# Optimization experiments

Hardware: AMD Instinct MI355X
Metric: run time of the kernel (lower is better)

Reference implementation:

```python
import jax, jax.numpy as jnp
import numpy as np

L, H, NH, NKV, HD, FF, E, K = 4, 1024, 16, 4, 64, 2048, 8, 2
B, S = 2, 2048
THETA, EPS = 10000.0, 1e-5


def setup_inputs() -> dict:
    key = jax.random.key(0)
    ks = jax.random.split(key, 12)
    sc = 0.02
    inp = {
        "hidden_states": jax.random.normal(ks[0], (B, S, H), jnp.float32),
        "ln1_w": jnp.ones((L, H), jnp.float32),
        "ln2_w": jnp.ones((L, H), jnp.float32),
        "wq": jax.random.normal(ks[1], (L, H, NH * HD), jnp.float32) * sc,
        "wk": jax.random.normal(ks[2], (L, H, NKV * HD), jnp.float32) * sc,
        "wv": jax.random.normal(ks[3], (L, H, NKV * HD), jnp.float32) * sc,
        "wo": jax.random.normal(ks[4], (L, NH * HD, H), jnp.float32) * sc,
        "wr": jax.random.normal(ks[5], (L, H, E), jnp.float32) * sc,
        "wg": jax.random.normal(ks[6], (L, E, H, FF), jnp.float32) * sc,
        "wu": jax.random.normal(ks[7], (L, E, H, FF), jnp.float32) * sc,
        "wd": jax.random.normal(ks[8], (L, E, FF, H), jnp.float32) * sc,
    }
    return inp


def _rms(x, w):
    return x * jax.lax.rsqrt(jnp.mean(x * x, axis=-1, keepdims=True) + EPS) * w


def _rope_cos_sin(seq_len, head_dim, theta):
    inv = 1.0 / (theta ** (jnp.arange(0, head_dim, 2, dtype=jnp.float32) / head_dim))
    f = jnp.arange(seq_len, dtype=jnp.float32)[:, None] * inv  # [S, HD/2]
    emb = jnp.concatenate([f, f], axis=-1)  # [S, HD]
    return jnp.cos(emb), jnp.sin(emb)


def _rot_half(x):
    h = x.shape[-1] // 2
    return jnp.concatenate([-x[..., h:], x[..., :h]], axis=-1)


def _attention(x, wq, wk, wv, wo, cos, sin, causal_bias):
    b, s, _ = x.shape
    q = (x @ wq).reshape(b, s, NH, HD).transpose(0, 2, 1, 3)   # [B,NH,S,HD]
    k = (x @ wk).reshape(b, s, NKV, HD).transpose(0, 2, 1, 3)  # [B,NKV,S,HD]
    v = (x @ wv).reshape(b, s, NKV, HD).transpose(0, 2, 1, 3)
    c = cos[None, None]
    sn = sin[None, None]
    q = q * c + _rot_half(q) * sn
    k = k * c + _rot_half(k) * sn
    rep = NH // NKV
    k = jnp.repeat(k, rep, axis=1)  # [B,NH,S,HD]
    v = jnp.repeat(v, rep, axis=1)
    scores = jnp.einsum("bhqd,bhkd->bhqk", q, k) / jnp.sqrt(jnp.asarray(HD, x.dtype))
    scores = scores + causal_bias  # [1,1,S,S] broadcast
    attn = jax.nn.softmax(scores, axis=-1)
    out = jnp.einsum("bhqk,bhkd->bhqd", attn, v)
    out = out.transpose(0, 2, 1, 3).reshape(b, s, NH * HD)
    return out @ wo


def _moe(x, wr, wg, wu, wd):
    logits = x @ wr                            # [B,S,E]
    probs = jax.nn.softmax(logits, axis=-1)
    topv, topi = jax.lax.top_k(probs, K)       # [B,S,K]
    topv = topv / jnp.sum(topv, axis=-1, keepdims=True)
    # dense per-expert combine weights [B,S,E]
    comb = jnp.sum(jax.nn.one_hot(topi, E, dtype=x.dtype) * topv[..., None], axis=-2)
    out = jnp.zeros_like(x)
    for e in range(E):  # fixed small expert count
        h = jax.nn.silu(x @ wg[e]) * (x @ wu[e])  # [B,S,FF]
        out = out + comb[..., e:e + 1] * (h @ wd[e])
    return out


def reference(hidden_states, ln1_w, ln2_w, wq, wk, wv, wo, wr, wg, wu, wd):
    s = hidden_states.shape[1]
    cos, sin = _rope_cos_sin(s, HD, THETA)
    causal_bias = jnp.where(
        jnp.tril(jnp.ones((s, s), bool))[None, None], 0.0, -1e9
    ).astype(hidden_states.dtype)
    x = hidden_states
    for l in range(L):
        res = x
        h = _rms(x, ln1_w[l])
        h = _attention(h, wq[l], wk[l], wv[l], wo[l], cos, sin, causal_bias)
        x = jnp.clip(res + h, -100.0, 100.0)
        res = x
        h = _rms(x, ln2_w[l])
        h = _moe(h, wr[l], wg[l], wu[l], wd[l])
        x = jnp.clip(res + h, -100.0, 100.0)
    return x
```

## Files before the change

kernel.cpp:

```cpp
#include <hip/hip_runtime.h>
#include <math.h>

typedef unsigned short u16;
typedef short short8 __attribute__((ext_vector_type(8)));
typedef short short4v __attribute__((ext_vector_type(4)));
typedef float f32x4 __attribute__((ext_vector_type(4)));

#define NLAYER 4
#define HDIM 1024
#define NHEAD 16
#define NKVH 4
#define FFDIM 2048
#define NEXP 8
#define SEQ 2048
#define NBATCH 2
#define NTOK (NBATCH*SEQ)
#define NPAIR (NTOK*2)
#define RMS_EPS 1e-5f

__device__ __forceinline__ u16 b16(float x) {
  unsigned u = __builtin_bit_cast(unsigned, x);
  unsigned r = (u + 0x7FFFu + ((u >> 16) & 1u)) >> 16;
  return (u16)r;
}
__device__ __forceinline__ float b2f(u16 b) {
  return __builtin_bit_cast(float, ((unsigned)b) << 16);
}
__device__ __forceinline__ void split2(float x, u16& o0, u16& o1) {
  o0 = b16(x); o1 = b16(x - b2f(o0));
}
__device__ __forceinline__ float clip100(float v) {
  return fminf(fmaxf(v, -100.f), 100.f);
}
__device__ __forceinline__ int swz8(int bid, int nwg) {
  return (bid & 7) * (nwg >> 3) + (bid >> 3);
}

__global__ __launch_bounds__(256)
void rmsnorm_kernel(const float* __restrict__ x, const float* __restrict__ w,
                    u16* __restrict__ oh, u16* __restrict__ ol) {
  int t = blockIdx.x, tid = threadIdx.x;
  const float* xr = x + (long)t * HDIM;
  float4 v = *(const float4*)(xr + tid * 4);
  float ss = v.x*v.x + v.y*v.y + v.z*v.z + v.w*v.w;
  #pragma unroll
  for (int m = 32; m; m >>= 1) ss += __shfl_xor(ss, m);
  __shared__ float sb[4];
  if ((tid & 63) == 0) sb[tid >> 6] = ss;
  __syncthreads();
  ss = sb[0] + sb[1] + sb[2] + sb[3];
  float sc = 1.0f / sqrtf(ss * (1.f/HDIM) + RMS_EPS);
  float4 wv = *(const float4*)(w + tid * 4);
  float ov[4] = {v.x*sc*wv.x, v.y*sc*wv.y, v.z*sc*wv.z, v.w*sc*wv.w};
  short4v hv, lv;
  #pragma unroll
  for (int j = 0; j < 4; j++) { u16 h, l; split2(ov[j], h, l); hv[j]=(short)h; lv[j]=(short)l; }
  *(short4v*)&oh[(long)t*HDIM + tid*4] = hv;
  *(short4v*)&ol[(long)t*HDIM + tid*4] = lv;
}

__global__ __launch_bounds__(256)
void rope_table_kernel(float* __restrict__ tab) {
  int idx = blockIdx.x * 256 + threadIdx.x;
  int i = idx & 31, pos = idx >> 5;
  double e = -(double)i * 0.28782313662425575;
  float inv = (float)exp(e);
  float f = (float)pos * inv;
  tab[idx] = cosf(f);
  tab[SEQ*32 + idx] = sinf(f);
}

#define GPAD 40

__device__ __forceinline__ void gemm_core(
    const u16* __restrict__ Ah, const u16* __restrict__ Al, long arow,
    const float* __restrict__ Bp, int Nb, int bcol0, int K,
    u16 (&As)[2][256][GPAD], u16 (&Bs)[2][64][GPAD],
    int tid, int wr, int lr, int lg, f32x4 (&acc)[4][4])
{
  int b_col = tid & 63;
  int b_kh = (tid >> 6) * 8;
  short8 pA[8];
  float pB[8];
  short8 cBh, cBl;
  auto loadA = [&](int k0) {
    if (arow >= 0) {
      const u16* ah = Ah + arow * (long)K + k0;
      const u16* al = Al + arow * (long)K + k0;
      #pragma unroll
      for (int q = 0; q < 4; q++) {
        pA[q]     = *(const short8*)(ah + q*8);
        pA[4 + q] = *(const short8*)(al + q*8);
      }
    } else {
      short8 z = {0,0,0,0,0,0,0,0};
      #pragma unroll
      for (int q = 0; q < 8; q++) pA[q] = z;
    }
  };
  auto loadB = [&](int k0) {
    const float* bp = Bp + (long)(k0 + b_kh) * Nb + bcol0 + b_col;
    #pragma unroll
    for (int j = 0; j < 8; j++) pB[j] = bp[(long)j * Nb];
  };
  auto convB = [&]() {
    #pragma unroll
    for (int j = 0; j < 8; j++) {
      u16 h, l; split2(pB[j], h, l);
      cBh[j] = (short)h; cBl[j] = (short)l;
    }
  };
  loadA(0); loadB(0); convB();
  for (int k0 = 0; k0 < K; k0 += 32) {
    if (k0) __syncthreads();
    #pragma unroll
    for (int q = 0; q < 4; q++) {
      *(short8*)&As[0][tid][q*8] = pA[q];
      *(short8*)&As[1][tid][q*8] = pA[4 + q];
    }
    *(short8*)&Bs[0][b_col][b_kh] = cBh;
    *(short8*)&Bs[1][b_col][b_kh] = cBl;
    __syncthreads();
    int kn = k0 + 32;
    if (kn < K) { loadA(kn); loadB(kn); }
    short8 bf[2][4];
    #pragma unroll
    for (int t = 0; t < 2; t++)
      #pragma unroll
      for (int n = 0; n < 4; n++)
        bf[t][n] = *(const short8*)&Bs[t][n*16 + lr][lg*8];
    #pragma unroll
    for (int m = 0; m < 4; m++) {
      short8 afh = *(const short8*)&As[0][wr + m*16 + lr][lg*8];
      short8 afl = *(const short8*)&As[1][wr + m*16 + lr][lg*8];
      #pragma unroll
      for (int n = 0; n < 4; n++) {
        f32x4 a = acc[m][n];
        a = __builtin_amdgcn_mfma_f32_16x16x32_bf16(afh, bf[0][n], a, 0, 0, 0);
        a = __builtin_amdgcn_mfma_f32_16x16x32_bf16(afh, bf[1][n], a, 0, 0, 0);
        a = __builtin_amdgcn_mfma_f32_16x16x32_bf16(afl, bf[0][n], a, 0, 0, 0);
        acc[m][n] = a;
      }
    }
    if (kn < K) convB();
  }
}

__device__ __forceinline__ void gemm_core128(
    const u16* __restrict__ Ah, const u16* __restrict__ Al, long arow,
    const float* __restrict__ Bp, int Nb, int bcol0, int K,
    u16 (&As)[2][128][GPAD], u16 (&Bs)[2][64][GPAD],
    int tid, int wr, int lr, int lg, f32x4 (&acc)[2][4])
{
  int a_r = tid >> 1, a_kq = (tid & 1) * 16;
  int b_col = tid & 63;
  int b_kh = (tid >> 6) * 8;
  short8 pA[4];
  float pB[8];
  short8 cBh, cBl;
  auto loadA = [&](int k0) {
    if (arow >= 0) {
      const u16* ah = Ah + arow * (long)K + k0 + a_kq;
      const u16* al = Al + arow * (long)K + k0 + a_kq;
      pA[0] = *(const short8*)ah;
      pA[1] = *(const short8*)(ah + 8);
      pA[2] = *(const short8*)al;
      pA[3] = *(const short8*)(al + 8);
    } else {
      short8 z = {0,0,0,0,0,0,0,0};
      #pragma unroll
      for (int q = 0; q < 4; q++) pA[q] = z;
    }
  };
  auto loadB = [&](int k0) {
    const float* bp = Bp + (long)(k0 + b_kh) * Nb + bcol0 + b_col;
    #pragma unroll
    for (int j = 0; j < 8; j++) pB[j] = bp[(long)j * Nb];
  };
  auto convB = [&]() {
    #pragma unroll
    for (int j = 0; j < 8; j++) {
      u16 h, l; split2(pB[j], h, l);
      cBh[j] = (short)h; cBl[j] = (short)l;
    }
  };
  loadA(0); loadB(0); convB();
  for (int k0 = 0; k0 < K; k0 += 32) {
    if (k0) __syncthreads();
    *(short8*)&As[0][a_r][a_kq]     = pA[0];
    *(short8*)&As[0][a_r][a_kq + 8] = pA[1];
    *(short8*)&As[1][a_r][a_kq]     = pA[2];
    *(short8*)&As[1][a_r][a_kq + 8] = pA[3];
    *(short8*)&Bs[0][b_col][b_kh] = cBh;
    *(short8*)&Bs[1][b_col][b_kh] = cBl;
    __syncthreads();
    int kn = k0 + 32;
    if (kn < K) { loadA(kn); loadB(kn); }
    short8 bf[2][4];
    #pragma unroll
    for (int t = 0; t < 2; t++)
      #pragma unroll
      for (int n = 0; n < 4; n++)
        bf[t][n] = *(const short8*)&Bs[t][n*16 + lr][lg*8];
    #pragma unroll
    for (int m = 0; m < 2; m++) {
      short8 afh = *(const short8*)&As[0][wr + m*16 + lr][lg*8];
      short8 afl = *(const short8*)&As[1][wr + m*16 + lr][lg*8];
      #pragma unroll
      for (int n = 0; n < 4; n++) {
        f32x4 a = acc[m][n];
        a = __builtin_amdgcn_mfma_f32_16x16x32_bf16(afh, bf[0][n], a, 0, 0, 0);
        a = __builtin_amdgcn_mfma_f32_16x16x32_bf16(afh, bf[1][n], a, 0, 0, 0);
        a = __builtin_amdgcn_mfma_f32_16x16x32_bf16(afl, bf[0][n], a, 0, 0, 0);
        acc[m][n] = a;
      }
    }
    if (kn < K) convB();
  }
}

__global__ __launch_bounds__(256)
void gemm_down(const u16* __restrict__ Ah, const u16* __restrict__ Al,
               const float* __restrict__ B, float* __restrict__ Cf,
               const int* __restrict__ offs, int N, int K, long bstride, int ncol)
{
  __shared__ u16 As[2][128][GPAD];
  __shared__ u16 Bs[2][64][GPAD];
  int nwg = gridDim.x;
  int bid = swz8(blockIdx.x, nwg);
  int cpe = nwg >> 3;
  int z = bid / cpe, rr2 = bid % cpe;
  int rs = offs[z], re = offs[z + 1];
  int brow = rr2 / ncol, bcol = rr2 % ncol;
  int p0 = rs + brow * 128;
  if (p0 >= re) return;
  int bcol0 = bcol * 64;
  const float* Bp = B + (long)z * bstride;
  int tid = threadIdx.x, wv = tid >> 6, lane = tid & 63;
  int lr = lane & 15, lg = lane >> 4;
  int wr = wv * 32;
  long arow = -1;
  { int rr = p0 + (tid >> 1); if (rr < re) arow = rr; }
  f32x4 acc[2][4];
  #pragma unroll
  for (int m = 0; m < 2; m++)
    #pragma unroll
    for (int n = 0; n < 4; n++) acc[m][n] = {0.f,0.f,0.f,0.f};
  gemm_core128(Ah, Al, arow, Bp, N, bcol0, K, As, Bs, tid, wr, lr, lg, acc);
  #pragma unroll
  for (int m = 0; m < 2; m++) {
    int row0 = p0 + wr + m*16 + lg*4;
    #pragma unroll
    for (int n = 0; n < 4; n++) {
      int col = bcol0 + n*16 + lr;
      #pragma unroll
      for (int r = 0; r < 4; r++) {
        int row = row0 + r;
        if (row < re) Cf[(long)row * N + col] = acc[m][n][r];
      }
    }
  }
}

__global__ __launch_bounds__(256)
void gemm_wo(const u16* __restrict__ Ah, const u16* __restrict__ Al,
             const float* __restrict__ B, float* __restrict__ Cf,
             int M, int N, int K, int ncol)
{
  __shared__ u16 As[2][128][GPAD];
  __shared__ u16 Bs[2][64][GPAD];
  int bid = swz8(blockIdx.x, gridDim.x);
  int brow = bid / ncol, bcol = bid % ncol;
  int p0 = brow * 128;
  int bcol0 = bcol * 64;
  int tid = threadIdx.x, wv = tid >> 6, lane = tid & 63;
  int lr = lane & 15, lg = lane >> 4;
  int wr = wv * 32;
  long arow = p0 + (tid >> 1);
  f32x4 acc[2][4];
  #pragma unroll
  for (int m = 0; m < 2; m++)
    #pragma unroll
    for (int n = 0; n < 4; n++) acc[m][n] = {0.f,0.f,0.f,0.f};
  gemm_core128(Ah, Al, arow, B, N, bcol0, K, As, Bs, tid, wr, lr, lg, acc);
  #pragma unroll
  for (int m = 0; m < 2; m++) {
    int row0 = p0 + wr + m*16 + lg*4;
    #pragma unroll
    for (int n = 0; n < 4; n++) {
      int col = bcol0 + n*16 + lr;
      #pragma unroll
      for (int r = 0; r < 4; r++) {
        long idx = (long)(row0 + r) * N + col;
        Cf[idx] = clip100(Cf[idx] + acc[m][n][r]);
      }
    }
  }
}

#define GUPAD 40
__global__ __launch_bounds__(256, 2)
void gemm_gateup(const u16* __restrict__ Ah, const u16* __restrict__ Al,
                 const float* __restrict__ Bg, const float* __restrict__ Bu,
                 u16* __restrict__ Ch, u16* __restrict__ Cl,
                 const int* __restrict__ gather, const int* __restrict__ offs)
{
  __shared__ u16 As[2][256][GUPAD];
  __shared__ u16 Bgs[2][64][GUPAD];
  __shared__ u16 Bus[2][64][GUPAD];
  const int K = HDIM, N = FFDIM;
  int nwg = gridDim.x;
  int bid = swz8(blockIdx.x, nwg);
  int cpe = nwg >> 3;
  int z = bid / cpe, rr2 = bid % cpe;
  int rs = offs[z], re = offs[z + 1];
  int brow = rr2 >> 5, bcol = rr2 & 31;
  int p0 = rs + brow * 256;
  if (p0 >= re) return;
  int bcol0 = bcol * 64;
  const float* Bpg = Bg + (long)z * ((long)HDIM * FFDIM);
  const float* Bpu = Bu + (long)z * ((long)HDIM * FFDIM);
  int tid = threadIdx.x, wv = tid >> 6, lane = tid & 63;
  int lr = lane & 15, lg = lane >> 4;
  int wr = wv * 64;
  long arow = -1;
  { int rr = p0 + tid; if (rr < re) arow = gather[rr]; }
  f32x4 accg[4][4], accu[4][4];
  #pragma unroll
  for (int m = 0; m < 4; m++)
    #pragma unroll
    for (int n = 0; n < 4; n++) { accg[m][n] = {0.f,0.f,0.f,0.f}; accu[m][n] = {0.f,0.f,0.f,0.f}; }
  int b_col = tid & 63;
  int b_kh = (tid >> 6) * 8;
  short8 pA[8];
  float pBg[8], pBu[8];
  short8 cGh, cGl, cUh, cUl;
  auto loadA = [&](int k0) {
    if (arow >= 0) {
      const u16* ah = Ah + arow * (long)K + k0;
      const u16* al = Al + arow * (long)K + k0;
      #pragma unroll
      for (int q = 0; q < 4; q++) {
        pA[q]     = *(const short8*)(ah + q*8);
        pA[4 + q] = *(const short8*)(al + q*8);
      }
    } else {
      short8 zz = {0,0,0,0,0,0,0,0};
      #pragma unroll
      for (int q = 0; q < 8; q++) pA[q] = zz;
    }
  };
  auto loadB = [&](int k0) {
    const float* bpg = Bpg + (long)(k0 + b_kh) * N + bcol0 + b_col;
    const float* bpu = Bpu + (long)(k0 + b_kh) * N + bcol0 + b_col;
    #pragma unroll
    for (int j = 0; j < 8; j++) { pBg[j] = bpg[(long)j * N]; pBu[j] = bpu[(long)j * N]; }
  };
  auto convB = [&]() {
    #pragma unroll
    for (int j = 0; j < 8; j++) {
      u16 h, l;
      split2(pBg[j], h, l); cGh[j] = (short)h; cGl[j] = (short)l;
      split2(pBu[j], h, l); cUh[j] = (short)h; cUl[j] = (short)l;
    }
  };
  loadA(0); loadB(0); convB();
  for (int k0 = 0; k0 < K; k0 += 32) {
    if (k0) __syncthreads();
    #pragma unroll
    for (int q = 0; q < 4; q++) {
      *(short8*)&As[0][tid][q*8] = pA[q];
      *(short8*)&As[1][tid][q*8] = pA[4 + q];
    }
    *(short8*)&Bgs[0][b_col][b_kh] = cGh;
    *(short8*)&Bgs[1][b_col][b_kh] = cGl;
    *(short8*)&Bus[0][b_col][b_kh] = cUh;
    *(short8*)&Bus[1][b_col][b_kh] = cUl;
    __syncthreads();
    int kn = k0 + 32;
    if (kn < K) { loadA(kn); loadB(kn); }
    short8 afh[4], afl[4];
    #pragma unroll
    for (int m = 0; m < 4; m++) {
      afh[m] = *(const short8*)&As[0][wr + m*16 + lr][lg*8];
      afl[m] = *(const short8*)&As[1][wr + m*16 + lr][lg*8];
    }
    #pragma unroll
    for (int n = 0; n < 4; n++) {
      short8 bgh = *(const short8*)&Bgs[0][n*16 + lr][lg*8];
      short8 bgl = *(const short8*)&Bgs[1][n*16 + lr][lg*8];
      short8 buh = *(const short8*)&Bus[0][n*16 + lr][lg*8];
      short8 bul = *(const short8*)&Bus[1][n*16 + lr][lg*8];
      #pragma unroll
      for (int m = 0; m < 4; m++) {
        f32x4 g = accg[m][n];
        g = __builtin_amdgcn_mfma_f32_16x16x32_bf16(afh[m], bgh, g, 0, 0, 0);
        g = __builtin_amdgcn_mfma_f32_16x16x32_bf16(afh[m], bgl, g, 0, 0, 0);
        g = __builtin_amdgcn_mfma_f32_16x16x32_bf16(afl[m], bgh, g, 0, 0, 0);
        accg[m][n] = g;
        f32x4 u = accu[m][n];
        u = __builtin_amdgcn_mfma_f32_16x16x32_bf16(afh[m], buh, u, 0, 0, 0);
        u = __builtin_amdgcn_mfma_f32_16x16x32_bf16(afh[m], bul, u, 0, 0, 0);
        u = __builtin_amdgcn_mfma_f32_16x16x32_bf16(afl[m], buh, u, 0, 0, 0);
        accu[m][n] = u;
      }
    }
    if (kn < K) convB();
  }
  #pragma unroll
  for (int m = 0; m < 4; m++) {
    int row0 = p0 + wr + m*16 + lg*4;
    #pragma unroll
    for (int n = 0; n < 4; n++) {
      int col = bcol0 + n*16 + lr;
      #pragma unroll
      for (int r = 0; r < 4; r++) {
        int row = row0 + r;
        if (row < re) {
          float gv = accg[m][n][r], uv = accu[m][n][r];
          float hh = gv / (1.f + __expf(-gv)) * uv;
          u16 h, l; split2(hh, h, l);
          long idx = (long)row * N + col;
          Ch[idx] = h; Cl[idx] = l;
        }
      }
    }
  }
}

__global__ __launch_bounds__(256)
void gemm_qkv(const u16* __restrict__ Ah, const u16* __restrict__ Al,
              const float* __restrict__ wq, const float* __restrict__ wk,
              const float* __restrict__ wv_, const float* __restrict__ tab,
              u16* __restrict__ qh, u16* __restrict__ ql,
              u16* __restrict__ kh_, u16* __restrict__ kl_,
              u16* __restrict__ vth, u16* __restrict__ vtl)
{
  __shared__ u16 As[2][128][GPAD];
  __shared__ u16 Bs[2][64][GPAD];
  int bid = swz8(blockIdx.x, gridDim.x);
  int bx = bid % 24;
  int p0 = (bid / 24) * 128;
  const float* Bp; int Nb, bcol0;
  if (bx < 16)      { Bp = wq;  Nb = 1024; bcol0 = bx * 64; }
  else if (bx < 20) { Bp = wk;  Nb = 256;  bcol0 = (bx - 16) * 64; }
  else              { Bp = wv_; Nb = 256;  bcol0 = (bx - 20) * 64; }
  int K = HDIM;
  int tid = threadIdx.x, wv = tid >> 6, lane = tid & 63;
  int lr = lane & 15, lg = lane >> 4;
  int wr = wv * 32;
  long arow = p0 + (tid >> 1);
  f32x4 acc[2][4];
  #pragma unroll
  for (int m = 0; m < 2; m++)
    #pragma unroll
    for (int n = 0; n < 4; n++) acc[m][n] = {0.f,0.f,0.f,0.f};
  gemm_core128(Ah, Al, arow, Bp, Nb, bcol0, K, As, Bs, tid, wr, lr, lg, acc);
  if (bx < 16) {
    int h = bx;
    #pragma unroll
    for (int m = 0; m < 2; m++) {
      #pragma unroll
      for (int r = 0; r < 4; r++) {
        int tok = p0 + wr + m*16 + lg*4 + r;
        int pos = tok & (SEQ - 1);
        #pragma unroll
        for (int n = 0; n < 2; n++) {
          int i = n*16 + lr;
          float c = tab[pos*32 + i], s = tab[SEQ*32 + pos*32 + i];
          float x0 = acc[m][n][r], x1 = acc[m][n+2][r];
          float y0 = x0*c - x1*s, y1 = x1*c + x0*s;
          long base = (long)tok*1024 + h*64 + i;
          u16 h0, l0; split2(y0, h0, l0); qh[base] = h0; ql[base] = l0;
          u16 h1, l1; split2(y1, h1, l1); qh[base+32] = h1; ql[base+32] = l1;
        }
      }
    }
  } else if (bx < 20) {
    int kvh = bx - 16;
    #pragma unroll
    for (int m = 0; m < 2; m++) {
      #pragma unroll
      for (int r = 0; r < 4; r++) {
        int tok = p0 + wr + m*16 + lg*4 + r;
        int pos = tok & (SEQ - 1);
        #pragma unroll
        for (int n = 0; n < 2; n++) {
          int i = n*16 + lr;
          float c = tab[pos*32 + i], s = tab[SEQ*32 + pos*32 + i];
          float x0 = acc[m][n][r], x1 = acc[m][n+2][r];
          float y0 = x0*c - x1*s, y1 = x1*c + x0*s;
          long base = (long)tok*256 + kvh*64 + i;
          u16 h0, l0; split2(y0, h0, l0); kh_[base] = h0; kl_[base] = l0;
          u16 h1, l1; split2(y1, h1, l1); kh_[base+32] = h1; kl_[base+32] = l1;
        }
      }
    }
  } else {
    int kvh = bx - 20;
    #pragma unroll
    for (int m = 0; m < 2; m++) {
      #pragma unroll
      for (int r = 0; r < 4; r++) {
        int tok = p0 + wr + m*16 + lg*4 + r;
        int bb = tok >> 11, tl = tok & (SEQ - 1);
        #pragma unroll
        for (int n = 0; n < 4; n++) {
          int hd = n*16 + lr;
          u16 h0, l0; split2(acc[m][n][r], h0, l0);
          long vidx = ((long)(bb*NKVH + kvh)*64 + hd)*SEQ + tl;
          vth[vidx] = h0; vtl[vidx] = l0;
        }
      }
    }
  }
}

#define ATP 70
#define PPAD 68
__global__ __launch_bounds__(256)
void attn_kernel(const u16* __restrict__ qhi, const u16* __restrict__ qlo,
                 const u16* __restrict__ khi, const u16* __restrict__ klo,
                 const u16* __restrict__ vthi, const u16* __restrict__ vtlo,
                 u16* __restrict__ ohi, u16* __restrict__ olo)
{
  int bid = swz8(blockIdx.x, gridDim.x);
  int qp = bid & 15, h = (bid >> 4) & 15, b = bid >> 8;
  int kvh = h >> 2;
  int tid = threadIdx.x, w = tid >> 6, lane = tid & 63;
  int lr = lane & 15, lg = lane >> 4;
  __shared__ u16 KhS[64][ATP], KlS[64][ATP], VhS[64][ATP], VlS[64][ATP];
  __shared__ u16 Ps[2][4][16][PPAD];
  long tokbase = (long)b * SEQ;
  int sr = tid >> 2, scg = (tid & 3) * 16;
  const u16* vrow_h = vthi + ((long)(b*NKVH + kvh)*64 + sr)*SEQ;
  const u16* vrow_l = vtlo + ((long)(b*NKVH + kvh)*64 + sr)*SEQ;
  short8 pK[4], pV[4];
  auto loadKV = [&](int kt) {
    long kg = (tokbase + kt*64 + sr)*256 + kvh*64 + scg;
    pK[0] = *(const short8*)(khi + kg);
    pK[1] = *(const short8*)(khi + kg + 8);
    pK[2] = *(const short8*)(klo + kg);
    pK[3] = *(const short8*)(klo + kg + 8);
    long vg = kt*64 + scg;
    pV[0] = *(const short8*)(vrow_h + vg);
    pV[1] = *(const short8*)(vrow_h + vg + 8);
    pV[2] = *(const short8*)(vrow_l + vg);
    pV[3] = *(const short8*)(vrow_l + vg + 8);
  };
  loadKV(0);

  for (int ph = 0; ph < 2; ph++) {
    int qt = ph ? (31 - qp) : qp;
    long q0 = (long)qt * 64;
    const u16* qh_row = qhi + (tokbase + q0 + w*16 + lr)*1024 + h*64;
    const u16* ql_row = qlo + (tokbase + q0 + w*16 + lr)*1024 + h*64;
    short8 aqh[2], aql[2];
    #pragma unroll
    for (int hf = 0; hf < 2; hf++) {
      aqh[hf] = *(const short8*)(qh_row + hf*32 + lg*8);
      aql[hf] = *(const short8*)(ql_row + hf*32 + lg*8);
    }
    f32x4 Oacc[4];
    #pragma unroll
    for (int n = 0; n < 4; n++) Oacc[n] = {0.f,0.f,0.f,0.f};
    float mrow[4] = {-1e30f,-1e30f,-1e30f,-1e30f};
    float lrow[4] = {0.f,0.f,0.f,0.f};
    for (int kt = 0; kt <= qt; kt++) {
      if (ph | kt) __syncthreads();
      *(short8*)&KhS[sr][scg]   = pK[0];
      *(short8*)&KhS[sr][scg+8] = pK[1];
      *(short8*)&KlS[sr][scg]   = pK[2];
      *(short8*)&KlS[sr][scg+8] = pK[3];
      *(short8*)&VhS[sr][scg]   = pV[0];
      *(short8*)&VhS[sr][scg+8] = pV[1];
      *(short8*)&VlS[sr][scg]   = pV[2];
      *(short8*)&VlS[sr][scg+8] = pV[3];
      __syncthreads();
      loadKV(kt < qt ? kt + 1 : 0);
      float sv[4][4];
      #pragma unroll
      for (int n = 0; n < 4; n++) {
        short8 bh0 = *(const short8*)&KhS[n*16 + lr][lg*8];
        short8 bh1 = *(const short8*)&KhS[n*16 + lr][32 + lg*8];
        short8 bl0 = *(const short8*)&KlS[n*16 + lr][lg*8];
        short8 bl1 = *(const short8*)&KlS[n*16 + lr][32 + lg*8];
        f32x4 c = {0.f,0.f,0.f,0.f};
        c = __builtin_amdgcn_mfma_f32_16x16x32_bf16(aqh[0], bh0, c, 0, 0, 0);
        c = __builtin_amdgcn_mfma_f32_16x16x32_bf16(aqh[1], bh1, c, 0, 0, 0);
        c = __builtin_amdgcn_mfma_f32_16x16x32_bf16(aqh[0], bl0, c, 0, 0, 0);
        c = __builtin_amdgcn_mfma_f32_16x16x32_bf16(aqh[1], bl1, c, 0, 0, 0);
        c = __builtin_amdgcn_mfma_f32_16x16x32_bf16(aql[0], bh0, c, 0, 0, 0);
        c = __builtin_amdgcn_mfma_f32_16x16x32_bf16(aql[1], bh1, c, 0, 0, 0);
        #pragma unroll
        for (int r = 0; r < 4; r++) sv[n][r] = c[r] * 0.125f;
      }
      if (kt == qt) {
        #pragma unroll
        for (int n = 0; n < 4; n++)
          #pragma unroll
          for (int r = 0; r < 4; r++)
            if (n*16 + lr > w*16 + lg*4 + r) sv[n][r] = -1e30f;
      }
      float pvv[4][4], alpha[4];
      #pragma unroll
      for (int r = 0; r < 4; r++) {
        float vm = fmaxf(fmaxf(sv[0][r], sv[1][r]), fmaxf(sv[2][r], sv[3][r]));
        #pragma unroll
        for (int msk = 1; msk < 16; msk <<= 1) vm = fmaxf(vm, __shfl_xor(vm, msk));
        float mnew = fmaxf(mrow[r], vm);
        alpha[r] = __expf(mrow[r] - mnew);
        float psum = 0.f;
        #pragma unroll
        for (int n = 0; n < 4; n++) { pvv[n][r] = __expf(sv[n][r] - mnew); psum += pvv[n][r]; }
        #pragma unroll
        for (int msk = 1; msk < 16; msk <<= 1) psum += __shfl_xor(psum, msk);
        lrow[r] = lrow[r] * alpha[r] + psum;
        mrow[r] = mnew;
      }
      #pragma unroll
      for (int n = 0; n < 4; n++)
        #pragma unroll
        for (int r = 0; r < 4; r++) {
          u16 t0, t1;
          split2(pvv[n][r], t0, t1);
          Ps[0][w][lg*4 + r][n*16 + lr] = t0;
          Ps[1][w][lg*4 + r][n*16 + lr] = t1;
        }
      #pragma unroll
      for (int n = 0; n < 4; n++)
        #pragma unroll
        for (int r = 0; r < 4; r++) Oacc[n][r] *= alpha[r];
      #pragma unroll
      for (int kk = 0; kk < 2; kk++) {
        short8 aph = *(const short8*)&Ps[0][w][lr][kk*32 + lg*8];
        short8 apl = *(const short8*)&Ps[1][w][lr][kk*32 + lg*8];
        #pragma unroll
        for (int n = 0; n < 4; n++) {
          short8 bvh = *(const short8*)&VhS[n*16 + lr][kk*32 + lg*8];
          short8 bvl = *(const short8*)&VlS[n*16 + lr][kk*32 + lg*8];
          f32x4 a = Oacc[n];
          a = __builtin_amdgcn_mfma_f32_16x16x32_bf16(aph, bvh, a, 0, 0, 0);
          a = __builtin_amdgcn_mfma_f32_16x16x32_bf16(aph, bvl, a, 0, 0, 0);
          a = __builtin_amdgcn_mfma_f32_16x16x32_bf16(apl, bvh, a, 0, 0, 0);
          Oacc[n] = a;
        }
      }
    }
    u16* oh_row = ohi + (tokbase + q0 + w*16)*1024 + h*64;
    u16* ol_row = olo + (tokbase + q0 + w*16)*1024 + h*64;
    #pragma unroll
    for (int n = 0; n < 4; n++)
      #pragma unroll
      for (int r = 0; r < 4; r++) {
        float v = Oacc[n][r] / lrow[r];
        u16 h0, l0; split2(v, h0, l0);
        oh_row[(lg*4 + r)*1024 + n*16 + lr] = h0;
        ol_row[(lg*4 + r)*1024 + n*16 + lr] = l0;
      }
  }
}

__global__ __launch_bounds__(64)
void router_kernel(const float* __restrict__ x, const float* __restrict__ w2,
                   const float* __restrict__ wr, int* __restrict__ tok_e,
                   float* __restrict__ tok_w, int* __restrict__ counts)
{
  int t = blockIdx.x, l = threadIdx.x;
  const float* xr = x + (long)t * HDIM;
  float xv[16];
  float ss = 0.f;
  #pragma unroll
  for (int j = 0; j < 16; j++) { xv[j] = xr[l + j*64]; ss += xv[j]*xv[j]; }
  #pragma unroll
  for (int m = 32; m; m >>= 1) ss += __shfl_xor(ss, m);
  float sc = 1.0f / sqrtf(ss * (1.f/HDIM) + RMS_EPS);
  float acc[8] = {0,0,0,0,0,0,0,0};
  #pragma unroll
  for (int j = 0; j < 16; j++) {
    int hh = l + j*64;
    float xnv = xv[j] * sc * w2[hh];
    const float* wrow = wr + hh * 8;
    #pragma unroll
    for (int e = 0; e < 8; e++) acc[e] += xnv * wrow[e];
  }
  #pragma unroll
  for (int e = 0; e < 8; e++)
    #pragma unroll
    for (int m = 32; m; m >>= 1) acc[e] += __shfl_xor(acc[e], m);
  if (l == 0) {
    float mx = acc[0];
    #pragma unroll
    for (int e = 1; e < 8; e++) mx = fmaxf(mx, acc[e]);
    float ex[8], s = 0.f;
    #pragma unroll
    for (int e = 0; e < 8; e++) { ex[e] = expf(acc[e] - mx); s += ex[e]; }
    int e0 = 0;
    #pragma unroll
    for (int e = 1; e < 8; e++) if (ex[e] > ex[e0]) e0 = e;
    int e1 = (e0 == 0) ? 1 : 0;
    for (int e = 0; e < 8; e++) if (e != e0 && ex[e] > ex[e1]) e1 = e;
    float v0 = ex[e0] / s, v1 = ex[e1] / s, wsum = v0 + v1;
    tok_e[2*t] = e0; tok_e[2*t+1] = e1;
    tok_w[2*t] = v0 / wsum; tok_w[2*t+1] = v1 / wsum;
    atomicAdd(&counts[e0], 1);
    atomicAdd(&counts[e1], 1);
  }
}

__global__ void scan_kernel(const int* __restrict__ counts, int* __restrict__ offs,
                            int* __restrict__ cursor) {
  if (threadIdx.x == 0 && blockIdx.x == 0) {
    int s = 0;
    for (int e = 0; e < NEXP; e++) { offs[e] = s; cursor[e] = s; s += counts[e]; }
    offs[NEXP] = s;
  }
}

__global__ __launch_bounds__(256)
void scatter_kernel(const int* __restrict__ tok_e, int* __restrict__ cursor,
                    int* __restrict__ tok_of_pair, int* __restrict__ tok_slot) {
  int t = blockIdx.x * 256 + threadIdx.x;
  if (t >= NTOK) return;
  #pragma unroll
  for (int s = 0; s < 2; s++) {
    int e = tok_e[2*t + s];
    int pos = atomicAdd(&cursor[e], 1);
    tok_of_pair[pos] = t;
    tok_slot[2*t + s] = pos;
  }
}

__global__ __launch_bounds__(256)
void combine_kernel(float* __restrict__ x, const float* __restrict__ po,
                    const int* __restrict__ tok_slot, const float* __restrict__ tok_w) {
  int t = blockIdx.x, tid = threadIdx.x;
  long s0 = tok_slot[2*t], s1 = tok_slot[2*t+1];
  float w0 = tok_w[2*t], w1 = tok_w[2*t+1];
  int c = tid * 4;
  float4 xv = *(float4*)(x + (long)t*HDIM + c);
  float4 a  = *(const float4*)(po + s0*HDIM + c);
  float4 bb = *(const float4*)(po + s1*HDIM + c);
  xv.x = clip100(xv.x + w0*a.x + w1*bb.x);
  xv.y = clip100(xv.y + w0*a.y + w1*bb.y);
  xv.z = clip100(xv.z + w0*a.z + w1*bb.z);
  xv.w = clip100(xv.w + w0*a.w + w1*bb.w);
  *(float4*)(x + (long)t*HDIM + c) = xv;
}

extern "C" void kernel_launch(void* const* d_in, const int* in_sizes, int n_in,
                              void* d_out, int out_size, void* d_ws, size_t ws_size,
                              hipStream_t stream)
{
  (void)in_sizes; (void)n_in; (void)out_size; (void)ws_size;
  const float* hs  = (const float*)d_in[0];
  const float* ln1 = (const float*)d_in[1];
  const float* ln2 = (const float*)d_in[2];
  const float* wq  = (const float*)d_in[3];
  const float* wk  = (const float*)d_in[4];
  const float* wvv = (const float*)d_in[5];
  const float* wo  = (const float*)d_in[6];
  const float* wr  = (const float*)d_in[7];
  const float* wg  = (const float*)d_in[8];
  const float* wu  = (const float*)d_in[9];
  const float* wd  = (const float*)d_in[10];
  float* x = (float*)d_out;

  char* p = (char*)d_ws;
  auto carve = [&](size_t bytes) {
    char* r = p; p += (bytes + 255) & ~(size_t)255; return r;
  };
  float* tab = (float*)carve((size_t)SEQ * 32 * 2 * 4);
  u16* xnh = (u16*)carve((size_t)NTOK * HDIM * 2);
  u16* xnl = (u16*)carve((size_t)NTOK * HDIM * 2);
  char* R  = carve((size_t)128 * 1024 * 1024);
  u16* qhi = (u16*)R;
  u16* qlo = (u16*)(R + 8u*1024*1024);
  u16* khi = (u16*)(R + 16u*1024*1024);
  u16* klo = (u16*)(R + 18u*1024*1024);
  u16* vthi= (u16*)(R + 20u*1024*1024);
  u16* vtlo= (u16*)(R + 22u*1024*1024);
  u16* ohi = (u16*)(R + 24u*1024*1024);
  u16* olo = (u16*)(R + 32u*1024*1024);
  u16*   ghi = (u16*)R;
  u16*   glo = (u16*)(R + 32u*1024*1024);
  float* po  = (float*)(R + 64u*1024*1024);
  int*   tok_e       = (int*)carve(NTOK * 2 * 4);
  float* tok_w       = (float*)carve(NTOK * 2 * 4);
  int*   tok_slot    = (int*)carve(NTOK * 2 * 4);
  int*   tok_of_pair = (int*)carve(NPAIR * 4);
  int*   counts      = (int*)carve(8 * 4);
  int*   offs        = (int*)carve(9 * 4);
  int*   cursor      = (int*)carve(8 * 4);

  hipMemcpyAsync(x, hs, (size_t)NTOK * HDIM * 4, hipMemcpyDeviceToDevice, stream);
  rope_table_kernel<<<SEQ*32/256, 256, 0, stream>>>(tab);

  for (int l = 0; l < NLAYER; l++) {
    rmsnorm_kernel<<<NTOK, 256, 0, stream>>>(x, ln1 + (long)l*HDIM, xnh, xnl);
    gemm_qkv<<<768, 256, 0, stream>>>(
        xnh, xnl, wq + (long)l*HDIM*1024, wk + (long)l*HDIM*256,
        wvv + (long)l*HDIM*256, tab, qhi, qlo, khi, klo, vthi, vtlo);
    attn_kernel<<<512, 256, 0, stream>>>(
        qhi, qlo, khi, klo, vthi, vtlo, ohi, olo);
    gemm_wo<<<512, 256, 0, stream>>>(
        ohi, olo, wo + (long)l*1024*HDIM, x, NTOK, HDIM, 1024, 16);

    rmsnorm_kernel<<<NTOK, 256, 0, stream>>>(x, ln2 + (long)l*HDIM, xnh, xnl);
    hipMemsetAsync(counts, 0, 8 * 4, stream);
    router_kernel<<<NTOK, 64, 0, stream>>>(
        x, ln2 + (long)l*HDIM, wr + (long)l*HDIM*NEXP, tok_e, tok_w, counts);
    scan_kernel<<<1, 64, 0, stream>>>(counts, offs, cursor);
    scatter_kernel<<<NTOK/256, 256, 0, stream>>>(tok_e, cursor, tok_of_pair, tok_slot);
    gemm_gateup<<<8192, 256, 0, stream>>>(
        xnh, xnl, wg + (long)l*NEXP*HDIM*FFDIM, wu + (long)l*NEXP*HDIM*FFDIM,
        ghi, glo, tok_of_pair, offs);
    gemm_down<<<8192, 256, 0, stream>>>(
        ghi, glo, wd + (long)l*NEXP*FFDIM*HDIM, po,
        offs, HDIM, FFDIM, (long)FFDIM*HDIM, 16);
    combine_kernel<<<NTOK, 256, 0, stream>>>(x, po, tok_slot, tok_w);
  }
}
```

Measured before the change: 3.604 ms.

## Pre-split weights into packed bf16 hi/lo words and double-buffer B prefetch

Adds a per-layer pass that converts every fp32 weight into a packed 32-bit word holding its bf16 high and low parts, so the GEMM inner loops only unpack bits instead of rounding and subtracting on each tile. The GEMM cores now keep two register stages of B (and A for the 128-row core), which prefetches two K-steps ahead. The unused 256-row gemm_core is removed. The split pass reads and writes all weights once per layer (about 200MB each way for the expert weights), and the extra prefetch buffers raise register pressure.

```diff
diff --git a/kernel.cpp b/kernel.cpp
--- a/kernel.cpp
+++ b/kernel.cpp
@@ -2,6 +2,7 @@
 #include <math.h>
 
 typedef unsigned short u16;
+typedef unsigned int u32t;
 typedef short short8 __attribute__((ext_vector_type(8)));
 typedef short short4v __attribute__((ext_vector_type(4)));
 typedef float f32x4 __attribute__((ext_vector_type(4)));
@@ -37,6 +38,22 @@
 }
 
 __global__ __launch_bounds__(256)
+void splitw_kernel(const float* __restrict__ src, u32t* __restrict__ dst, long n) {
+  long i = ((long)blockIdx.x * 256 + threadIdx.x) * 4;
+  if (i >= n) return;
+  float4 v = *(const float4*)(src + i);
+  float vv[4] = {v.x, v.y, v.z, v.w};
+  u32t o[4];
+  #pragma unroll
+  for (int j = 0; j < 4; j++) {
+    u16 h, l; split2(vv[j], h, l);
+    o[j] = ((u32t)h << 16) | (u32t)l;
+  }
+  uint4 ov; ov.x = o[0]; ov.y = o[1]; ov.z = o[2]; ov.w = o[3];
+  *(uint4*)&dst[i] = ov;
+}
+
+__global__ __launch_bounds__(256)
 void rmsnorm_kernel(const float* __restrict__ x, const float* __restrict__ w,
                     u16* __restrict__ oh, u16* __restrict__ ol) {
   int t = blockIdx.x, tid = threadIdx.x;
@@ -72,156 +89,84 @@
 
 #define GPAD 40
 
-__device__ __forceinline__ void gemm_core(
-    const u16* __restrict__ Ah, const u16* __restrict__ Al, long arow,
-    const float* __restrict__ Bp, int Nb, int bcol0, int K,
-    u16 (&As)[2][256][GPAD], u16 (&Bs)[2][64][GPAD],
-    int tid, int wr, int lr, int lg, f32x4 (&acc)[4][4])
-{
-  int b_col = tid & 63;
-  int b_kh = (tid >> 6) * 8;
-  short8 pA[8];
-  float pB[8];
-  short8 cBh, cBl;
-  auto loadA = [&](int k0) {
-    if (arow >= 0) {
-      const u16* ah = Ah + arow * (long)K + k0;
-      const u16* al = Al + arow * (long)K + k0;
-      #pragma unroll
-      for (int q = 0; q < 4; q++) {
-        pA[q]     = *(const short8*)(ah + q*8);
-        pA[4 + q] = *(const short8*)(al + q*8);
-      }
-    } else {
-      short8 z = {0,0,0,0,0,0,0,0};
-      #pragma unroll
-      for (int q = 0; q < 8; q++) pA[q] = z;
-    }
-  };
-  auto loadB = [&](int k0) {
-    const float* bp = Bp + (long)(k0 + b_kh) * Nb + bcol0 + b_col;
-    #pragma unroll
-    for (int j = 0; j < 8; j++) pB[j] = bp[(long)j * Nb];
-  };
-  auto convB = [&]() {
-    #pragma unroll
-    for (int j = 0; j < 8; j++) {
-      u16 h, l; split2(pB[j], h, l);
-      cBh[j] = (short)h; cBl[j] = (short)l;
-    }
-  };
-  loadA(0); loadB(0); convB();
-  for (int k0 = 0; k0 < K; k0 += 32) {
-    if (k0) __syncthreads();
-    #pragma unroll
-    for (int q = 0; q < 4; q++) {
-      *(short8*)&As[0][tid][q*8] = pA[q];
-      *(short8*)&As[1][tid][q*8] = pA[4 + q];
-    }
-    *(short8*)&Bs[0][b_col][b_kh] = cBh;
-    *(short8*)&Bs[1][b_col][b_kh] = cBl;
-    __syncthreads();
-    int kn = k0 + 32;
-    if (kn < K) { loadA(kn); loadB(kn); }
-    short8 bf[2][4];
-    #pragma unroll
-    for (int t = 0; t < 2; t++)
-      #pragma unroll
-      for (int n = 0; n < 4; n++)
-        bf[t][n] = *(const short8*)&Bs[t][n*16 + lr][lg*8];
-    #pragma unroll
-    for (int m = 0; m < 4; m++) {
-      short8 afh = *(const short8*)&As[0][wr + m*16 + lr][lg*8];
-      short8 afl = *(const short8*)&As[1][wr + m*16 + lr][lg*8];
-      #pragma unroll
-      for (int n = 0; n < 4; n++) {
-        f32x4 a = acc[m][n];
-        a = __builtin_amdgcn_mfma_f32_16x16x32_bf16(afh, bf[0][n], a, 0, 0, 0);
-        a = __builtin_amdgcn_mfma_f32_16x16x32_bf16(afh, bf[1][n], a, 0, 0, 0);
-        a = __builtin_amdgcn_mfma_f32_16x16x32_bf16(afl, bf[0][n], a, 0, 0, 0);
-        acc[m][n] = a;
-      }
-    }
-    if (kn < K) convB();
-  }
-}
+#define C128_STEP(s, cur)                                                      \
+  {                                                                            \
+    short8 bh, bl;                                                             \
+    _Pragma("unroll") for (int j = 0; j < 8; j++) {                            \
+      u32t wrd = pB[cur][j];                                                   \
+      bh[j] = (short)(u16)(wrd >> 16);                                         \
+      bl[j] = (short)(u16)(wrd & 0xffffu);                                     \
+    }                                                                          \
+    if (s) __syncthreads();                                                    \
+    *(short8*)&As[0][a_r][a_kq]     = pA[cur][0];                              \
+    *(short8*)&As[0][a_r][a_kq + 8] = pA[cur][1];                              \
+    *(short8*)&As[1][a_r][a_kq]     = pA[cur][2];                              \
+    *(short8*)&As[1][a_r][a_kq + 8] = pA[cur][3];                              \
+    *(short8*)&Bs[0][b_col][b_kh] = bh;                                        \
+    *(short8*)&Bs[1][b_col][b_kh] = bl;                                        \
+    __syncthreads();                                                           \
+    if ((s) + 2 < ns) {                                                        \
+      loadA(32*((s)+2), cur);                                                  \
+      loadB(32*((s)+2), cur);                                                  \
+    }                                                                          \
+    short8 bf[2][4];                                                           \
+    _Pragma("unroll") for (int t = 0; t < 2; t++)                              \
+      _Pragma("unroll") for (int n = 0; n < 4; n++)                            \
+        bf[t][n] = *(const short8*)&Bs[t][n*16 + lr][lg*8];                    \
+    _Pragma("unroll") for (int m = 0; m < 2; m++) {                            \
+      short8 afh = *(const short8*)&As[0][wr + m*16 + lr][lg*8];               \
+      short8 afl = *(const short8*)&As[1][wr + m*16 + lr][lg*8];               \
+      _Pragma("unroll") for (int n = 0; n < 4; n++) {                          \
+        f32x4 a = acc[m][n];                                                   \
+        a = __builtin_amdgcn_mfma_f32_16x16x32_bf16(afh, bf[0][n], a, 0, 0, 0);\
+        a = __builtin_amdgcn_mfma_f32_16x16x32_bf16(afh, bf[1][n], a, 0, 0, 0);\
+        a = __builtin_amdgcn_mfma_f32_16x16x32_bf16(afl, bf[0][n], a, 0, 0, 0);\
+        acc[m][n] = a;                                                         \
+      }                                                                        \
+    }                                                                          \
+  }
 
 __device__ __forceinline__ void gemm_core128(
     const u16* __restrict__ Ah, const u16* __restrict__ Al, long arow,
-    const float* __restrict__ Bp, int Nb, int bcol0, int K,
+    const u32t* __restrict__ Bw, int Nb, int bcol0, int K,
     u16 (&As)[2][128][GPAD], u16 (&Bs)[2][64][GPAD],
     int tid, int wr, int lr, int lg, f32x4 (&acc)[2][4])
 {
   int a_r = tid >> 1, a_kq = (tid & 1) * 16;
   int b_col = tid & 63;
   int b_kh = (tid >> 6) * 8;
-  short8 pA[4];
-  float pB[8];
-  short8 cBh, cBl;
-  auto loadA = [&](int k0) {
+  short8 pA[2][4];
+  u32t pB[2][8];
+  auto loadA = [&](int k0, int buf) {
     if (arow >= 0) {
       const u16* ah = Ah + arow * (long)K + k0 + a_kq;
       const u16* al = Al + arow * (long)K + k0 + a_kq;
-      pA[0] = *(const short8*)ah;
-      pA[1] = *(const short8*)(ah + 8);
-      pA[2] = *(const short8*)al;
-      pA[3] = *(const short8*)(al + 8);
+      pA[buf][0] = *(const short8*)ah;
+      pA[buf][1] = *(const short8*)(ah + 8);
+      pA[buf][2] = *(const short8*)al;
+      pA[buf][3] = *(const short8*)(al + 8);
     } else {
       short8 z = {0,0,0,0,0,0,0,0};
-      #pragma unroll
-      for (int q = 0; q < 4; q++) pA[q] = z;
+      pA[buf][0] = z; pA[buf][1] = z; pA[buf][2] = z; pA[buf][3] = z;
     }
   };
-  auto loadB = [&](int k0) {
-    const float* bp = Bp + (long)(k0 + b_kh) * Nb + bcol0 + b_col;
-    #pragma unroll
-    for (int j = 0; j < 8; j++) pB[j] = bp[(long)j * Nb];
+  auto loadB = [&](int k0, int buf) {
+    const u32t* bp = Bw + (long)(k0 + b_kh) * Nb + bcol0 + b_col;
+    #pragma unroll
+    for (int j = 0; j < 8; j++) pB[buf][j] = bp[(long)j * Nb];
   };
-  auto convB = [&]() {
-    #pragma unroll
-    for (int j = 0; j < 8; j++) {
-      u16 h, l; split2(pB[j], h, l);
-      cBh[j] = (short)h; cBl[j] = (short)l;
-    }
-  };
-  loadA(0); loadB(0); convB();
-  for (int k0 = 0; k0 < K; k0 += 32) {
-    if (k0) __syncthreads();
-    *(short8*)&As[0][a_r][a_kq]     = pA[0];
-    *(short8*)&As[0][a_r][a_kq + 8] = pA[1];
-    *(short8*)&As[1][a_r][a_kq]     = pA[2];
-    *(short8*)&As[1][a_r][a_kq + 8] = pA[3];
-    *(short8*)&Bs[0][b_col][b_kh] = cBh;
-    *(short8*)&Bs[1][b_col][b_kh] = cBl;
-    __syncthreads();
-    int kn = k0 + 32;
-    if (kn < K) { loadA(kn); loadB(kn); }
-    short8 bf[2][4];
-    #pragma unroll
-    for (int t = 0; t < 2; t++)
-      #pragma unroll
-      for (int n = 0; n < 4; n++)
-        bf[t][n] = *(const short8*)&Bs[t][n*16 + lr][lg*8];
-    #pragma unroll
-    for (int m = 0; m < 2; m++) {
-      short8 afh = *(const short8*)&As[0][wr + m*16 + lr][lg*8];
-      short8 afl = *(const short8*)&As[1][wr + m*16 + lr][lg*8];
-      #pragma unroll
-      for (int n = 0; n < 4; n++) {
-        f32x4 a = acc[m][n];
-        a = __builtin_amdgcn_mfma_f32_16x16x32_bf16(afh, bf[0][n], a, 0, 0, 0);
-        a = __builtin_amdgcn_mfma_f32_16x16x32_bf16(afh, bf[1][n], a, 0, 0, 0);
-        a = __builtin_amdgcn_mfma_f32_16x16x32_bf16(afl, bf[0][n], a, 0, 0, 0);
-        acc[m][n] = a;
-      }
-    }
-    if (kn < K) convB();
+  int ns = K >> 5;
+  loadA(0, 0); loadB(0, 0);
+  loadA(32, 1); loadB(32, 1);
+  for (int s = 0; s < ns; s += 2) {
+    C128_STEP(s, 0)
+    C128_STEP(s + 1, 1)
   }
 }
 
 __global__ __launch_bounds__(256)
 void gemm_down(const u16* __restrict__ Ah, const u16* __restrict__ Al,
-               const float* __restrict__ B, float* __restrict__ Cf,
+               const u32t* __restrict__ Bw, float* __restrict__ Cf,
                const int* __restrict__ offs, int N, int K, long bstride, int ncol)
 {
   __shared__ u16 As[2][128][GPAD];
@@ -235,7 +180,7 @@
   int p0 = rs + brow * 128;
   if (p0 >= re) return;
   int bcol0 = bcol * 64;
-  const float* Bp = B + (long)z * bstride;
+  const u32t* Bp = Bw + (long)z * bstride;
   int tid = threadIdx.x, wv = tid >> 6, lane = tid & 63;
   int lr = lane & 15, lg = lane >> 4;
   int wr = wv * 32;
@@ -264,7 +209,7 @@
 
 __global__ __launch_bounds__(256)
 void gemm_wo(const u16* __restrict__ Ah, const u16* __restrict__ Al,
-             const float* __restrict__ B, float* __restrict__ Cf,
+             const u32t* __restrict__ Bw, float* __restrict__ Cf,
              int M, int N, int K, int ncol)
 {
   __shared__ u16 As[2][128][GPAD];
@@ -282,7 +227,7 @@
   for (int m = 0; m < 2; m++)
     #pragma unroll
     for (int n = 0; n < 4; n++) acc[m][n] = {0.f,0.f,0.f,0.f};
-  gemm_core128(Ah, Al, arow, B, N, bcol0, K, As, Bs, tid, wr, lr, lg, acc);
+  gemm_core128(Ah, Al, arow, Bw, N, bcol0, K, As, Bs, tid, wr, lr, lg, acc);
   #pragma unroll
   for (int m = 0; m < 2; m++) {
     int row0 = p0 + wr + m*16 + lg*4;
@@ -299,9 +244,54 @@
 }
 
 #define GUPAD 40
+#define GU_STEP(s, cur)                                                        \
+  {                                                                            \
+    short8 gh, gl, uh, ul;                                                     \
+    _Pragma("unroll") for (int j = 0; j < 8; j++) {                            \
+      u32t wg_ = pBg[cur][j], wu_ = pBu[cur][j];                               \
+      gh[j] = (short)(u16)(wg_ >> 16); gl[j] = (short)(u16)(wg_ & 0xffffu);    \
+      uh[j] = (short)(u16)(wu_ >> 16); ul[j] = (short)(u16)(wu_ & 0xffffu);    \
+    }                                                                          \
+    if (s) __syncthreads();                                                    \
+    _Pragma("unroll") for (int q = 0; q < 4; q++) {                            \
+      *(short8*)&As[0][tid][q*8] = pA[q];                                      \
+      *(short8*)&As[1][tid][q*8] = pA[4 + q];                                  \
+    }                                                                          \
+    *(short8*)&Bgs[0][b_col][b_kh] = gh;                                       \
+    *(short8*)&Bgs[1][b_col][b_kh] = gl;                                       \
+    *(short8*)&Bus[0][b_col][b_kh] = uh;                                       \
+    *(short8*)&Bus[1][b_col][b_kh] = ul;                                       \
+    __syncthreads();                                                           \
+    if ((s) + 1 < ns) loadA(32*((s)+1));                                       \
+    if ((s) + 2 < ns) loadB(32*((s)+2), cur);                                  \
+    short8 afh[4], afl[4];                                                     \
+    _Pragma("unroll") for (int m = 0; m < 4; m++) {                            \
+      afh[m] = *(const short8*)&As[0][wr + m*16 + lr][lg*8];                   \
+      afl[m] = *(const short8*)&As[1][wr + m*16 + lr][lg*8];                   \
+    }                                                                          \
+    _Pragma("unroll") for (int n = 0; n < 4; n++) {                            \
+      short8 bgh = *(const short8*)&Bgs[0][n*16 + lr][lg*8];                   \
+      short8 bgl = *(const short8*)&Bgs[1][n*16 + lr][lg*8];                   \
+      short8 buh = *(const short8*)&Bus[0][n*16 + lr][lg*8];                   \
+      short8 bul = *(const short8*)&Bus[1][n*16 + lr][lg*8];                   \
+      _Pragma("unroll") for (int m = 0; m < 4; m++) {                          \
+        f32x4 g = accg[m][n];                                                  \
+        g = __builtin_amdgcn_mfma_f32_16x16x32_bf16(afh[m], bgh, g, 0, 0, 0);  \
+        g = __builtin_amdgcn_mfma_f32_16x16x32_bf16(afh[m], bgl, g, 0, 0, 0);  \
+        g = __builtin_amdgcn_mfma_f32_16x16x32_bf16(afl[m], bgh, g, 0, 0, 0);  \
+        accg[m][n] = g;                                                        \
+        f32x4 u = accu[m][n];                                                  \
+        u = __builtin_amdgcn_mfma_f32_16x16x32_bf16(afh[m], buh, u, 0, 0, 0);  \
+        u = __builtin_amdgcn_mfma_f32_16x16x32_bf16(afh[m], bul, u, 0, 0, 0);  \
+        u = __builtin_amdgcn_mfma_f32_16x16x32_bf16(afl[m], buh, u, 0, 0, 0);  \
+        accu[m][n] = u;                                                        \
+      }                                                                        \
+    }                                                                          \
+  }
+
 __global__ __launch_bounds__(256, 2)
 void gemm_gateup(const u16* __restrict__ Ah, const u16* __restrict__ Al,
-                 const float* __restrict__ Bg, const float* __restrict__ Bu,
+                 const u32t* __restrict__ Bg, const u32t* __restrict__ Bu,
                  u16* __restrict__ Ch, u16* __restrict__ Cl,
                  const int* __restrict__ gather, const int* __restrict__ offs)
 {
@@ -318,8 +308,8 @@
   int p0 = rs + brow * 256;
   if (p0 >= re) return;
   int bcol0 = bcol * 64;
-  const float* Bpg = Bg + (long)z * ((long)HDIM * FFDIM);
-  const float* Bpu = Bu + (long)z * ((long)HDIM * FFDIM);
+  const u32t* Bpg = Bg + (long)z * ((long)HDIM * FFDIM);
+  const u32t* Bpu = Bu + (long)z * ((long)HDIM * FFDIM);
   int tid = threadIdx.x, wv = tid >> 6, lane = tid & 63;
   int lr = lane & 15, lg = lane >> 4;
   int wr = wv * 64;
@@ -333,8 +323,7 @@
   int b_col = tid & 63;
   int b_kh = (tid >> 6) * 8;
   short8 pA[8];
-  float pBg[8], pBu[8];
-  short8 cGh, cGl, cUh, cUl;
+  u32t pBg[2][8], pBu[2][8];
   auto loadA = [&](int k0) {
     if (arow >= 0) {
       const u16* ah = Ah + arow * (long)K + k0;
@@ -350,62 +339,21 @@
       for (int q = 0; q < 8; q++) pA[q] = zz;
     }
   };
-  auto loadB = [&](int k0) {
-    const float* bpg = Bpg + (long)(k0 + b_kh) * N + bcol0 + b_col;
-    const float* bpu = Bpu + (long)(k0 + b_kh) * N + bcol0 + b_col;
-    #pragma unroll
-    for (int j = 0; j < 8; j++) { pBg[j] = bpg[(long)j * N]; pBu[j] = bpu[(long)j * N]; }
+  auto loadB = [&](int k0, int buf) {
+    const u32t* bpg = Bpg + (long)(k0 + b_kh) * N + bcol0 + b_col;
+    const u32t* bpu = Bpu + (long)(k0 + b_kh) * N + bcol0 + b_col;
+    #pragma unroll
+    for (int j = 0; j < 8; j++) {
+      pBg[buf][j] = bpg[(long)j * N];
+      pBu[buf][j] = bpu[(long)j * N];
+    }
   };
-  auto convB = [&]() {
-    #pragma unroll
-    for (int j = 0; j < 8; j++) {
-      u16 h, l;
-      split2(pBg[j], h, l); cGh[j] = (short)h; cGl[j] = (short)l;
-      split2(pBu[j], h, l); cUh[j] = (short)h; cUl[j] = (short)l;
-    }
-  };
-  loadA(0); loadB(0); convB();
-  for (int k0 = 0; k0 < K; k0 += 32) {
-    if (k0) __syncthreads();
-    #pragma unroll
-    for (int q = 0; q < 4; q++) {
-      *(short8*)&As[0][tid][q*8] = pA[q];
-      *(short8*)&As[1][tid][q*8] = pA[4 + q];
-    }
-    *(short8*)&Bgs[0][b_col][b_kh] = cGh;
-    *(short8*)&Bgs[1][b_col][b_kh] = cGl;
-    *(short8*)&Bus[0][b_col][b_kh] = cUh;
-    *(short8*)&Bus[1][b_col][b_kh] = cUl;
-    __syncthreads();
-    int kn = k0 + 32;
-    if (kn < K) { loadA(kn); loadB(kn); }
-    short8 afh[4], afl[4];
-    #pragma unroll
-    for (int m = 0; m < 4; m++) {
-      afh[m] = *(const short8*)&As[0][wr + m*16 + lr][lg*8];
-      afl[m] = *(const short8*)&As[1][wr + m*16 + lr][lg*8];
-    }
-    #pragma unroll
-    for (int n = 0; n < 4; n++) {
-      short8 bgh = *(const short8*)&Bgs[0][n*16 + lr][lg*8];
-      short8 bgl = *(const short8*)&Bgs[1][n*16 + lr][lg*8];
-      short8 buh = *(const short8*)&Bus[0][n*16 + lr][lg*8];
-      short8 bul = *(const short8*)&Bus[1][n*16 + lr][lg*8];
-      #pragma unroll
-      for (int m = 0; m < 4; m++) {
-        f32x4 g = accg[m][n];
-        g = __builtin_amdgcn_mfma_f32_16x16x32_bf16(afh[m], bgh, g, 0, 0, 0);
-        g = __builtin_amdgcn_mfma_f32_16x16x32_bf16(afh[m], bgl, g, 0, 0, 0);
-        g = __builtin_amdgcn_mfma_f32_16x16x32_bf16(afl[m], bgh, g, 0, 0, 0);
-        accg[m][n] = g;
-        f32x4 u = accu[m][n];
-        u = __builtin_amdgcn_mfma_f32_16x16x32_bf16(afh[m], buh, u, 0, 0, 0);
-        u = __builtin_amdgcn_mfma_f32_16x16x32_bf16(afh[m], bul, u, 0, 0, 0);
-        u = __builtin_amdgcn_mfma_f32_16x16x32_bf16(afl[m], buh, u, 0, 0, 0);
-        accu[m][n] = u;
-      }
-    }
-    if (kn < K) convB();
+  int ns = K >> 5;
+  loadA(0);
+  loadB(0, 0); loadB(32, 1);
+  for (int s = 0; s < ns; s += 2) {
+    GU_STEP(s, 0)
+    GU_STEP(s + 1, 1)
   }
   #pragma unroll
   for (int m = 0; m < 4; m++) {
@@ -430,8 +378,8 @@
 
 __global__ __launch_bounds__(256)
 void gemm_qkv(const u16* __restrict__ Ah, const u16* __restrict__ Al,
-              const float* __restrict__ wq, const float* __restrict__ wk,
-              const float* __restrict__ wv_, const float* __restrict__ tab,
+              const u32t* __restrict__ wq, const u32t* __restrict__ wk,
+              const u32t* __restrict__ wv_, const float* __restrict__ tab,
               u16* __restrict__ qh, u16* __restrict__ ql,
               u16* __restrict__ kh_, u16* __restrict__ kl_,
               u16* __restrict__ vth, u16* __restrict__ vtl)
@@ -441,7 +389,7 @@
   int bid = swz8(blockIdx.x, gridDim.x);
   int bx = bid % 24;
   int p0 = (bid / 24) * 128;
-  const float* Bp; int Nb, bcol0;
+  const u32t* Bp; int Nb, bcol0;
   if (bx < 16)      { Bp = wq;  Nb = 1024; bcol0 = bx * 64; }
   else if (bx < 20) { Bp = wk;  Nb = 256;  bcol0 = (bx - 16) * 64; }
   else              { Bp = wv_; Nb = 256;  bcol0 = (bx - 20) * 64; }
@@ -785,6 +733,13 @@
   u16*   ghi = (u16*)R;
   u16*   glo = (u16*)(R + 32u*1024*1024);
   float* po  = (float*)(R + 64u*1024*1024);
+  u32t* swq = (u32t*)carve((size_t)HDIM * 1024 * 4);
+  u32t* swk = (u32t*)carve((size_t)HDIM * 256 * 4);
+  u32t* swv = (u32t*)carve((size_t)HDIM * 256 * 4);
+  u32t* swo = (u32t*)carve((size_t)1024 * HDIM * 4);
+  u32t* swg = (u32t*)carve((size_t)NEXP * HDIM * FFDIM * 4);
+  u32t* swu = (u32t*)carve((size_t)NEXP * HDIM * FFDIM * 4);
+  u32t* swd = (u32t*)carve((size_t)NEXP * FFDIM * HDIM * 4);
   int*   tok_e       = (int*)carve(NTOK * 2 * 4);
   float* tok_w       = (float*)carve(NTOK * 2 * 4);
   int*   tok_slot    = (int*)carve(NTOK * 2 * 4);
@@ -796,15 +751,26 @@
   hipMemcpyAsync(x, hs, (size_t)NTOK * HDIM * 4, hipMemcpyDeviceToDevice, stream);
   rope_table_kernel<<<SEQ*32/256, 256, 0, stream>>>(tab);
 
+  auto SPL = [&](const float* s, u32t* d, long n) {
+    splitw_kernel<<<(int)((n/4 + 255)/256), 256, 0, stream>>>(s, d, n);
+  };
+
   for (int l = 0; l < NLAYER; l++) {
+    SPL(wq  + (long)l*HDIM*1024, swq, (long)HDIM*1024);
+    SPL(wk  + (long)l*HDIM*256,  swk, (long)HDIM*256);
+    SPL(wvv + (long)l*HDIM*256,  swv, (long)HDIM*256);
+    SPL(wo  + (long)l*1024*HDIM, swo, (long)1024*HDIM);
+    SPL(wg  + (long)l*NEXP*HDIM*FFDIM, swg, (long)NEXP*HDIM*FFDIM);
+    SPL(wu  + (long)l*NEXP*HDIM*FFDIM, swu, (long)NEXP*HDIM*FFDIM);
+    SPL(wd  + (long)l*NEXP*FFDIM*HDIM, swd, (long)NEXP*FFDIM*HDIM);
+
     rmsnorm_kernel<<<NTOK, 256, 0, stream>>>(x, ln1 + (long)l*HDIM, xnh, xnl);
     gemm_qkv<<<768, 256, 0, stream>>>(
-        xnh, xnl, wq + (long)l*HDIM*1024, wk + (long)l*HDIM*256,
-        wvv + (long)l*HDIM*256, tab, qhi, qlo, khi, klo, vthi, vtlo);
+        xnh, xnl, swq, swk, swv, tab, qhi, qlo, khi, klo, vthi, vtlo);
     attn_kernel<<<512, 256, 0, stream>>>(
         qhi, qlo, khi, klo, vthi, vtlo, ohi, olo);
     gemm_wo<<<512, 256, 0, stream>>>(
-        ohi, olo, wo + (long)l*1024*HDIM, x, NTOK, HDIM, 1024, 16);
+        ohi, olo, swo, x, NTOK, HDIM, 1024, 16);
 
     rmsnorm_kernel<<<NTOK, 256, 0, stream>>>(x, ln2 + (long)l*HDIM, xnh, xnl);
     hipMemsetAsync(counts, 0, 8 * 4, stream);
@@ -813,11 +779,9 @@
     scan_kernel<<<1, 64, 0, stream>>>(counts, offs, cursor);
     scatter_kernel<<<NTOK/256, 256, 0, stream>>>(tok_e, cursor, tok_of_pair, tok_slot);
     gemm_gateup<<<8192, 256, 0, stream>>>(
-        xnh, xnl, wg + (long)l*NEXP*HDIM*FFDIM, wu + (long)l*NEXP*HDIM*FFDIM,
-        ghi, glo, tok_of_pair, offs);
+        xnh, xnl, swg, swu, ghi, glo, tok_of_pair, offs);
     gemm_down<<<8192, 256, 0, stream>>>(
-        ghi, glo, wd + (long)l*NEXP*FFDIM*HDIM, po,
-        offs, HDIM, FFDIM, (long)FFDIM*HDIM, 16);
+        ghi, glo, swd, po, offs, HDIM, FFDIM, (long)FFDIM*HDIM, 16);
     combine_kernel<<<NTOK, 256, 0, stream>>>(x, po, tok_slot, tok_w);
   }
 }
```

Measured after the change: 4.477 ms. 1.24x slower.
